# Kernel optimization log

Measured on AMD Instinct MI355X. Metric: run time of the kernel, lower is better.

The kernel has to match this reference:

```python
import jax, jax.numpy as jnp
import numpy as np
from jax import lax

B, L, DM = 2, 1024, 1024
DIN, DSTATE, DCONV, DTRANK = 2048, 16, 4, 64


def setup_inputs() -> dict:
    key = jax.random.key(0)
    ks = jax.random.split(key, 8)
    s = 0.02
    x = jax.random.normal(ks[0], (B, L, DM), jnp.float32)
    in_proj_w = jax.random.normal(ks[1], (2 * DIN, DM), jnp.float32) * s
    conv_w = jax.random.normal(ks[2], (DIN, 1, DCONV), jnp.float32) * 0.2
    conv_b = jnp.zeros((DIN,), jnp.float32)
    x_proj_w = jax.random.normal(ks[3], (DTRANK + 2 * DSTATE, DIN), jnp.float32) * s
    dt_proj_w = jax.random.normal(ks[4], (DIN, DTRANK), jnp.float32) * s
    dt_proj_b = jnp.full((DIN,), -4.0, jnp.float32)  # small init dt after softplus
    # S4D-real init: A_log = log(1..d_state) per channel
    A_log = jnp.log(jnp.broadcast_to(jnp.arange(1, DSTATE + 1, dtype=jnp.float32), (DIN, DSTATE)))
    D_skip = jnp.ones((DIN,), jnp.float32)
    out_proj_w = jax.random.normal(ks[5], (DM, DIN), jnp.float32) * s
    return {
        "x": x, "norm_w": jnp.ones((DM,), jnp.float32), "norm_b": jnp.zeros((DM,), jnp.float32),
        "in_proj_w": in_proj_w, "conv_w": conv_w, "conv_b": conv_b,
        "x_proj_w": x_proj_w, "dt_proj_w": dt_proj_w, "dt_proj_b": dt_proj_b,
        "A_log": A_log, "D_skip": D_skip, "out_proj_w": out_proj_w,
    }


def _layernorm(x, w, b, eps=1e-5):
    mu = jnp.mean(x, axis=-1, keepdims=True)
    var = jnp.mean(jnp.square(x - mu), axis=-1, keepdims=True)
    return (x - mu) * lax.rsqrt(var + eps) * w + b


def _mamba(h, in_proj_w, conv_w, conv_b, x_proj_w, dt_proj_w, dt_proj_b, A_log, D_skip, out_proj_w):
    # h: [B, L, DM]
    xz = jnp.einsum('bld,ed->ble', h, in_proj_w)          # [B, L, 2*DIN]
    xm, z = jnp.split(xz, 2, axis=-1)                     # each [B, L, DIN]
    # causal depthwise conv1d over time
    xc = jnp.transpose(xm, (0, 2, 1))                     # [B, DIN, L]
    xc = jnp.pad(xc, ((0, 0), (0, 0), (DCONV - 1, 0)))
    xc = lax.conv_general_dilated(xc, conv_w, (1,), 'VALID',
                                  dimension_numbers=('NCH', 'OIH', 'NCH'),
                                  feature_group_count=DIN)
    xc = xc + conv_b[None, :, None]
    xc = jnp.transpose(xc, (0, 2, 1))                     # [B, L, DIN]
    xc = jax.nn.silu(xc)
    # input-dependent SSM parameters
    x_dbl = jnp.einsum('bld,ed->ble', xc, x_proj_w)       # [B, L, DTRANK+2N]
    dt, Bm, Cm = jnp.split(x_dbl, [DTRANK, DTRANK + DSTATE], axis=-1)
    dt = jax.nn.softplus(jnp.einsum('blr,dr->bld', dt, dt_proj_w) + dt_proj_b)  # [B, L, DIN]
    A = -jnp.exp(A_log)                                   # [DIN, N]
    deltaA = jnp.exp(dt[..., None] * A)                   # [B, L, DIN, N]
    deltaBu = dt[..., None] * Bm[:, :, None, :] * xc[..., None]  # [B, L, DIN, N]
    # sequential selective scan over time
    dA_t = jnp.transpose(deltaA, (1, 0, 2, 3))            # [L, B, DIN, N]
    dBu_t = jnp.transpose(deltaBu, (1, 0, 2, 3))
    C_t = jnp.transpose(Cm, (1, 0, 2))                    # [L, B, N]

    def step(hs, inp):
        dA, dBu, Ct = inp
        hs = dA * hs + dBu                                # [B, DIN, N]
        y = jnp.einsum('bdn,bn->bd', hs, Ct)
        return hs, y

    h0 = jnp.zeros((B, DIN, DSTATE), xc.dtype)
    _, ys = lax.scan(step, h0, (dA_t, dBu_t, C_t))        # ys: [L, B, DIN]
    y = jnp.transpose(ys, (1, 0, 2)) + xc * D_skip        # [B, L, DIN]
    y = y * jax.nn.silu(z)
    return jnp.einsum('bld,ed->ble', y, out_proj_w)       # [B, L, DM]


def reference(x, norm_w, norm_b, in_proj_w, conv_w, conv_b, x_proj_w,
              dt_proj_w, dt_proj_b, A_log, D_skip, out_proj_w):
    h = _layernorm(x, norm_w, norm_b)
    return x + _mamba(h, in_proj_w, conv_w, conv_b, x_proj_w,
                      dt_proj_w, dt_proj_b, A_log, D_skip, out_proj_w)
```

## Files before the change

### kernel.cpp

```cpp
#include <hip/hip_runtime.h>


typedef unsigned short u16;
typedef unsigned int u32;

typedef __bf16 bf16x8 __attribute__((ext_vector_type(8)));
typedef float f32x4 __attribute__((ext_vector_type(4)));

#define SCAN_G 32
#define SCAN_T 32
#define NSTATE 65536

#if __has_builtin(__builtin_amdgcn_exp2f)
#define EXP2F(x) __builtin_amdgcn_exp2f(x)
#else
#define EXP2F(x) exp2f(x)
#endif
#define LOG2E 1.44269504f

__device__ __forceinline__ u16 f2bf(float f) {
  u32 u = __float_as_uint(f);
  u32 r = u + 0x7FFFu + ((u >> 16) & 1u);
  return (u16)(r >> 16);
}
__device__ __forceinline__ float bf2f(u16 v) {
  return __uint_as_float(((u32)v) << 16);
}

__device__ __forceinline__ void lds_load16(const u16* g, u16* l) {
  __builtin_amdgcn_global_load_lds(
      (const __attribute__((address_space(1))) u32*)g,
      (__attribute__((address_space(3))) u32*)l, 16, 0, 0);
}

__global__ __launch_bounds__(256) void convert_all_kernel(
    const float* __restrict__ w0, const float* __restrict__ w1,
    const float* __restrict__ w2, const float* __restrict__ w3,
    u16* __restrict__ o0, u16* __restrict__ o1,
    u16* __restrict__ o2, u16* __restrict__ o3) {
  const int i = blockIdx.x * 256 + threadIdx.x;
  if (i < 4194304) {
    o0[i] = f2bf(w0[i]);
  } else if (i < 4390912) {
    const int j = i - 4194304;
    o1[j] = f2bf(w1[j]);
  } else if (i < 4521984) {
    const int j = i - 4390912;
    o2[j] = f2bf(w2[j]);
  } else if (i < 6619136) {
    const int j = i - 4521984;
    o3[j] = f2bf(w3[j]);
  }
}

__global__ __launch_bounds__(256) void ln_bf16_kernel(
    const float* __restrict__ x, const float* __restrict__ w,
    const float* __restrict__ b, u16* __restrict__ h) {
  const int row = blockIdx.x;
  const int tid = threadIdx.x;
  const float4 v = ((const float4*)(x + (size_t)row * 1024))[tid];
  float s = v.x + v.y + v.z + v.w;
  float s2 = v.x * v.x + v.y * v.y + v.z * v.z + v.w * v.w;
  for (int off = 32; off >= 1; off >>= 1) {
    s += __shfl_xor(s, off);
    s2 += __shfl_xor(s2, off);
  }
  __shared__ float red[8];
  const int wave = tid >> 6;
  if ((tid & 63) == 0) { red[wave * 2] = s; red[wave * 2 + 1] = s2; }
  __syncthreads();
  s = red[0] + red[2] + red[4] + red[6];
  s2 = red[1] + red[3] + red[5] + red[7];
  const float mu = s * (1.0f / 1024.0f);
  const float var = s2 * (1.0f / 1024.0f) - mu * mu;
  const float rstd = rsqrtf(var + 1e-5f);
  const float4 wv = ((const float4*)w)[tid];
  const float4 bv = ((const float4*)b)[tid];
  ushort4 o;
  o.x = f2bf((v.x - mu) * rstd * wv.x + bv.x);
  o.y = f2bf((v.y - mu) * rstd * wv.y + bv.y);
  o.z = f2bf((v.z - mu) * rstd * wv.z + bv.z);
  o.w = f2bf((v.w - mu) * rstd * wv.w + bv.w);
  ((ushort4*)(h + (size_t)row * 1024))[tid] = o;
}

template <int EPI, int SPLITK>
__global__ __launch_bounds__(256) void gemm_bt(
    const u16* __restrict__ A, const u16* __restrict__ W,
    void* __restrict__ C, const float* __restrict__ extra,
    int M, int N, int K) {
  const int n0 = blockIdx.x * 64;
  const int m0 = blockIdx.y * 64;
  const int ks = (SPLITK > 1) ? blockIdx.z : 0;
  const int kLen = K / SPLITK;
  const int kOff = ks * kLen;
  __shared__ u16 As[64 * 32];
  __shared__ u16 Ws[64 * 32];
  const int tid = threadIdx.x;
  const int wave = tid >> 6;
  const int lane = tid & 63;
  const int wm = (wave >> 1) * 32;
  const int wn = (wave & 1) * 32;
  const int lrow = tid >> 2;
  const int lcg = (tid & 3) * 8;
  const int arow = m0 + lrow;
  const int wrow = n0 + lrow;
  f32x4 acc[2][2];
#pragma unroll
  for (int i = 0; i < 2; ++i)
#pragma unroll
    for (int j = 0; j < 2; ++j) acc[i][j] = (f32x4){0.f, 0.f, 0.f, 0.f};

  const int fm = lane & 15;
  const int fk = (lane >> 4) * 8;

  for (int k0 = kOff; k0 < kOff + kLen; k0 += 32) {
    uint4 av = *(const uint4*)(A + (size_t)arow * K + k0 + lcg);
    uint4 wv = make_uint4(0u, 0u, 0u, 0u);
    if (wrow < N) wv = *(const uint4*)(W + (size_t)wrow * K + k0 + lcg);
    __syncthreads();
    *(uint4*)(As + lrow * 32 + lcg) = av;
    *(uint4*)(Ws + lrow * 32 + lcg) = wv;
    __syncthreads();
    bf16x8 a0 = *(const bf16x8*)(As + (wm + fm) * 32 + fk);
    bf16x8 a1 = *(const bf16x8*)(As + (wm + 16 + fm) * 32 + fk);
    bf16x8 b0 = *(const bf16x8*)(Ws + (wn + fm) * 32 + fk);
    bf16x8 b1 = *(const bf16x8*)(Ws + (wn + 16 + fm) * 32 + fk);
    acc[0][0] = __builtin_amdgcn_mfma_f32_16x16x32_bf16(a0, b0, acc[0][0], 0, 0, 0);
    acc[0][1] = __builtin_amdgcn_mfma_f32_16x16x32_bf16(a0, b1, acc[0][1], 0, 0, 0);
    acc[1][0] = __builtin_amdgcn_mfma_f32_16x16x32_bf16(a1, b0, acc[1][0], 0, 0, 0);
    acc[1][1] = __builtin_amdgcn_mfma_f32_16x16x32_bf16(a1, b1, acc[1][1], 0, 0, 0);
  }

  const int col = lane & 15;
  const int rbase = (lane >> 4) * 4;
#pragma unroll
  for (int tm = 0; tm < 2; ++tm)
#pragma unroll
    for (int tn = 0; tn < 2; ++tn)
#pragma unroll
      for (int r = 0; r < 4; ++r) {
        int m = m0 + wm + tm * 16 + rbase + r;
        int n = n0 + wn + tn * 16 + col;
        if (n < N) {
          float v = acc[tm][tn][r];
          if (EPI == 0) {
            ((float*)C)[(size_t)ks * M * N + (size_t)m * N + n] = v;
          } else {
            v += extra[n];
            v = (v > 20.f) ? v : log1pf(__expf(v));
            ((u16*)C)[(size_t)m * N + n] = f2bf(v);
          }
        }
      }
}

template <int EPI, int SPLITK>
__global__ __launch_bounds__(256) void gemm128_kernel(
    const u16* __restrict__ A, const u16* __restrict__ W,
    u16* __restrict__ Cout, int M, int N, int K) {
  const int n0 = blockIdx.x * 128;
  const int m0 = blockIdx.y * 128;
  const int ks = (SPLITK > 1) ? blockIdx.z : 0;
  const int kLen = K / SPLITK;
  const int k0 = ks * kLen;
  __shared__ u16 As[128 * 32];
  __shared__ u16 Ws[128 * 32];
  const int tid = threadIdx.x;
  const int wave = tid >> 6;
  const int lane = tid & 63;
  const int wm = (wave >> 1) * 64;
  const int wn = (wave & 1) * 64;
  f32x4 acc[4][4];
#pragma unroll
  for (int i = 0; i < 4; ++i)
#pragma unroll
    for (int j = 0; j < 4; ++j) acc[i][j] = (f32x4){0.f, 0.f, 0.f, 0.f};

  const int fm = lane & 15;
  const int fk = (lane >> 4) * 8;
  const int sr = lane >> 2;
  const int sc = (lane & 3) * 8;
  const u16* gA = A + (size_t)(m0 + wave * 32 + sr) * K + k0 + sc;
  const u16* gB = W + (size_t)(n0 + wave * 32 + sr) * K + k0 + sc;
  u16* lA = As + wave * 1024;
  u16* lB = Ws + wave * 1024;

  for (int kk = 0; kk < kLen; kk += 32) {
    __syncthreads();
    lds_load16(gA + kk, lA);
    lds_load16(gA + (size_t)16 * K + kk, lA + 512);
    lds_load16(gB + kk, lB);
    lds_load16(gB + (size_t)16 * K + kk, lB + 512);
    __syncthreads();
    bf16x8 af[4], bfr[4];
#pragma unroll
    for (int i = 0; i < 4; ++i)
      af[i] = *(const bf16x8*)(As + (wm + i * 16 + fm) * 32 + fk);
#pragma unroll
    for (int j = 0; j < 4; ++j)
      bfr[j] = *(const bf16x8*)(Ws + (wn + j * 16 + fm) * 32 + fk);
#pragma unroll
    for (int i = 0; i < 4; ++i)
#pragma unroll
      for (int j = 0; j < 4; ++j)
        acc[i][j] = __builtin_amdgcn_mfma_f32_16x16x32_bf16(af[i], bfr[j], acc[i][j], 0, 0, 0);
  }

  const int col = lane & 15;
  const int rb = (lane >> 4) * 4;
#pragma unroll
  for (int i = 0; i < 4; ++i)
#pragma unroll
    for (int j = 0; j < 4; ++j)
#pragma unroll
      for (int r = 0; r < 4; ++r) {
        const int m = m0 + wm + i * 16 + rb + r;
        const int n = n0 + wn + j * 16 + col;
        if (EPI == 4)
          Cout[(size_t)m * N + n] = f2bf(acc[i][j][r]);
        else
          Cout[(size_t)ks * M * N + (size_t)m * N + n] = f2bf(acc[i][j][r]);
      }
}

__global__ __launch_bounds__(256) void xproj_comb_kernel(
    const float* __restrict__ part, float* __restrict__ xdbl,
    u16* __restrict__ dtr) {
  const int i = blockIdx.x * 256 + threadIdx.x;
  const float v = part[i] + part[i + 196608] + part[i + 2 * 196608] +
                  part[i + 3 * 196608];
  xdbl[i] = v;
  const int m = i / 96;
  const int c = i - m * 96;
  if (c < 64) dtr[(size_t)m * 64 + c] = f2bf(v);
}

__global__ __launch_bounds__(256) void out_comb_kernel(
    const u16* __restrict__ part, const float* __restrict__ x,
    float* __restrict__ out) {
  const int i4 = (blockIdx.x * 256 + threadIdx.x) * 4;
  const float4 xv = *(const float4*)&x[i4];
  float a0 = xv.x, a1 = xv.y, a2 = xv.z, a3 = xv.w;
#pragma unroll
  for (int ks = 0; ks < 4; ++ks) {
    ushort4 pv = *(const ushort4*)&part[(size_t)ks * 2097152 + i4];
    a0 += bf2f(pv.x); a1 += bf2f(pv.y); a2 += bf2f(pv.z); a3 += bf2f(pv.w);
  }
  float4 o = {a0, a1, a2, a3};
  *(float4*)&out[i4] = o;
}

__global__ __launch_bounds__(256) void conv_silu_kernel(
    const u16* __restrict__ xzb, const float* __restrict__ cw,
    const float* __restrict__ cb, u16* __restrict__ xcb) {
  const int idx = blockIdx.x * 256 + threadIdx.x;
  const int d = idx & 2047;
  const int m = idx >> 11;
  const int l = m & 1023;
  const float4 wv = ((const float4*)cw)[d];
  const float w4[4] = {wv.x, wv.y, wv.z, wv.w};
  float acc = cb[d];
#pragma unroll
  for (int k = 0; k < 4; ++k) {
    int lk = l + k - 3;
    if (lk >= 0) acc += bf2f(xzb[(size_t)(m + k - 3) * 4096 + d]) * w4[k];
  }
  const float sv = acc / (1.0f + __expf(-acc));
  xcb[idx] = f2bf(sv);
}


__global__ __launch_bounds__(256) void scan_pass1_kernel(
    const u16* __restrict__ dtb, const u16* __restrict__ xcb,
    const float* __restrict__ xdbl, const float* __restrict__ A_log,
    float* __restrict__ hend, float* __restrict__ prodA) {
  const int bx = blockIdx.x;
  const int d0 = (bx & 7) * 256;
  const int b = (bx >> 3) & 1;
  const int g = bx >> 4;
  const int tid = threadIdx.x;
  const int d = d0 + tid;
  const int mb = b * 1024 + g * SCAN_T;

  float a2[16];
#pragma unroll
  for (int q = 0; q < 4; ++q) {
    float4 al = *(const float4*)&A_log[(size_t)d * 16 + q * 4];
    a2[q * 4 + 0] = -__expf(al.x) * LOG2E;
    a2[q * 4 + 1] = -__expf(al.y) * LOG2E;
    a2[q * 4 + 2] = -__expf(al.z) * LOG2E;
    a2[q * 4 + 3] = -__expf(al.w) * LOG2E;
  }

  __shared__ u32 sdx[SCAN_T][256];

#pragma unroll
  for (int i = tid * 4; i < SCAN_T * 256; i += 1024) {
    const int s = i >> 8, dl = i & 255;
    ushort4 d4 = *(const ushort4*)&dtb[(size_t)(mb + s) * 2048 + d0 + dl];
    ushort4 x4 = *(const ushort4*)&xcb[(size_t)(mb + s) * 2048 + d0 + dl];
    uint4 pk;
    pk.x = (u32)d4.x | ((u32)x4.x << 16);
    pk.y = (u32)d4.y | ((u32)x4.y << 16);
    pk.z = (u32)d4.z | ((u32)x4.z << 16);
    pk.w = (u32)d4.w | ((u32)x4.w << 16);
    *(uint4*)&sdx[s][dl] = pk;
  }
  __syncthreads();

  float h[16];
#pragma unroll
  for (int n = 0; n < 16; ++n) h[n] = 0.f;
  float cs = 0.f;

  for (int s = 0; s < SCAN_T; ++s) {
    const u32 u = sdx[s][tid];
    const float dtv = __uint_as_float(u << 16);
    const float xcv = __uint_as_float(u & 0xFFFF0000u);
    const float du = dtv * xcv;
    const float* Brow = xdbl + (size_t)(mb + s) * 96 + 64;
    const float4 B0 = *(const float4*)(Brow + 0);
    const float4 B1 = *(const float4*)(Brow + 4);
    const float4 B2 = *(const float4*)(Brow + 8);
    const float4 B3 = *(const float4*)(Brow + 12);
    const float Bv[16] = {B0.x, B0.y, B0.z, B0.w, B1.x, B1.y, B1.z, B1.w,
                          B2.x, B2.y, B2.z, B2.w, B3.x, B3.y, B3.z, B3.w};
#pragma unroll
    for (int n = 0; n < 16; ++n) {
      const float da = EXP2F(dtv * a2[n]);
      h[n] = __builtin_fmaf(da, h[n], du * Bv[n]);
    }
    cs += dtv;
  }

  const size_t base = ((size_t)(g * 2 + b) * 2048 + d) * 16;
#pragma unroll
  for (int q = 0; q < 4; ++q) {
    float4 hv = {h[q * 4], h[q * 4 + 1], h[q * 4 + 2], h[q * 4 + 3]};
    *(float4*)&hend[base + q * 4] = hv;
    float4 pv = {EXP2F(a2[q * 4] * cs), EXP2F(a2[q * 4 + 1] * cs),
                 EXP2F(a2[q * 4 + 2] * cs), EXP2F(a2[q * 4 + 3] * cs)};
    *(float4*)&prodA[base + q * 4] = pv;
  }
}

__global__ __launch_bounds__(256) void scan_combine_kernel(
    const float* __restrict__ hend, const float* __restrict__ prodA,
    float* __restrict__ hinit) {
  const int sid = blockIdx.x * 256 + threadIdx.x;
  float H = 0.f;
#pragma unroll 8
  for (int g = 0; g < SCAN_G; ++g) {
    hinit[g * NSTATE + sid] = H;
    H = prodA[g * NSTATE + sid] * H + hend[g * NSTATE + sid];
  }
}

__global__ __launch_bounds__(256) void scan_pass2_kernel(
    const u16* __restrict__ dtb, const u16* __restrict__ xcb,
    const u16* __restrict__ xzb, const float* __restrict__ xdbl,
    const float* __restrict__ A_log, const float* __restrict__ Dsk,
    const float* __restrict__ hinit, u16* __restrict__ yb) {
  const int bx = blockIdx.x;
  const int d0 = (bx & 7) * 256;
  const int b = (bx >> 3) & 1;
  const int g = bx >> 4;
  const int tid = threadIdx.x;
  const int d = d0 + tid;
  const int mb = b * 1024 + g * SCAN_T;

  float a2[16];
#pragma unroll
  for (int q = 0; q < 4; ++q) {
    float4 al = *(const float4*)&A_log[(size_t)d * 16 + q * 4];
    a2[q * 4 + 0] = -__expf(al.x) * LOG2E;
    a2[q * 4 + 1] = -__expf(al.y) * LOG2E;
    a2[q * 4 + 2] = -__expf(al.z) * LOG2E;
    a2[q * 4 + 3] = -__expf(al.w) * LOG2E;
  }
  const float Dd = Dsk[d];

  __shared__ u32 sdx[SCAN_T][256];
  __shared__ u16 sz[SCAN_T][256];

#pragma unroll
  for (int i = tid * 4; i < SCAN_T * 256; i += 1024) {
    const int s = i >> 8, dl = i & 255;
    ushort4 d4 = *(const ushort4*)&dtb[(size_t)(mb + s) * 2048 + d0 + dl];
    ushort4 x4 = *(const ushort4*)&xcb[(size_t)(mb + s) * 2048 + d0 + dl];
    uint4 pk;
    pk.x = (u32)d4.x | ((u32)x4.x << 16);
    pk.y = (u32)d4.y | ((u32)x4.y << 16);
    pk.z = (u32)d4.z | ((u32)x4.z << 16);
    pk.w = (u32)d4.w | ((u32)x4.w << 16);
    *(uint4*)&sdx[s][dl] = pk;
    *(ushort4*)&sz[s][dl] =
        *(const ushort4*)&xzb[(size_t)(mb + s) * 4096 + 2048 + d0 + dl];
  }
  __syncthreads();

  float h[16];
  {
    const float* hi = hinit + ((size_t)(g * 2 + b) * 2048 + d) * 16;
#pragma unroll
    for (int q = 0; q < 4; ++q) {
      float4 hv = *(const float4*)(hi + q * 4);
      h[q * 4] = hv.x; h[q * 4 + 1] = hv.y; h[q * 4 + 2] = hv.z; h[q * 4 + 3] = hv.w;
    }
  }

  for (int s = 0; s < SCAN_T; ++s) {
    const u32 u = sdx[s][tid];
    const float dtv = __uint_as_float(u << 16);
    const float xcv = __uint_as_float(u & 0xFFFF0000u);
    const float du = dtv * xcv;
    const float* Xrow = xdbl + (size_t)(mb + s) * 96 + 64;
    const float4 B0 = *(const float4*)(Xrow + 0);
    const float4 B1 = *(const float4*)(Xrow + 4);
    const float4 B2 = *(const float4*)(Xrow + 8);
    const float4 B3 = *(const float4*)(Xrow + 12);
    const float4 C0 = *(const float4*)(Xrow + 16);
    const float4 C1 = *(const float4*)(Xrow + 20);
    const float4 C2 = *(const float4*)(Xrow + 24);
    const float4 C3 = *(const float4*)(Xrow + 28);
    const float Bv[16] = {B0.x, B0.y, B0.z, B0.w, B1.x, B1.y, B1.z, B1.w,
                          B2.x, B2.y, B2.z, B2.w, B3.x, B3.y, B3.z, B3.w};
    const float Cv[16] = {C0.x, C0.y, C0.z, C0.w, C1.x, C1.y, C1.z, C1.w,
                          C2.x, C2.y, C2.z, C2.w, C3.x, C3.y, C3.z, C3.w};
    float y = 0.f;
#pragma unroll
    for (int n = 0; n < 16; ++n) {
      const float da = EXP2F(dtv * a2[n]);
      h[n] = __builtin_fmaf(da, h[n], du * Bv[n]);
      y = __builtin_fmaf(h[n], Cv[n], y);
    }
    const float zv = bf2f(sz[s][tid]);
    const float sig = 1.0f / (1.0f + EXP2F(-zv * LOG2E));
    const float yv = (y + xcv * Dd) * (zv * sig);
    yb[(size_t)(mb + s) * 2048 + d] = f2bf(yv);
  }
}

extern "C" void kernel_launch(void* const* d_in, const int* in_sizes, int n_in,
                              void* d_out, int out_size, void* d_ws, size_t ws_size,
                              hipStream_t stream) {
  const float* x        = (const float*)d_in[0];
  const float* norm_w   = (const float*)d_in[1];
  const float* norm_b   = (const float*)d_in[2];
  const float* in_projw = (const float*)d_in[3];
  const float* conv_w   = (const float*)d_in[4];
  const float* conv_b   = (const float*)d_in[5];
  const float* x_projw  = (const float*)d_in[6];
  const float* dt_projw = (const float*)d_in[7];
  const float* dt_projb = (const float*)d_in[8];
  const float* A_log    = (const float*)d_in[9];
  const float* D_skip   = (const float*)d_in[10];
  const float* out_projw= (const float*)d_in[11];
  float* out = (float*)d_out;

  char* p = (char*)d_ws;
  auto alloc = [&](size_t bytes) {
    char* r = p;
    p += (bytes + 255) & ~(size_t)255;
    return r;
  };
  u16* xzb    = (u16*)alloc(2048ULL * 4096 * 2);
  u16* xcb    = (u16*)alloc(2048ULL * 2048 * 2);
  u16* dtb16  = (u16*)alloc(2048ULL * 2048 * 2);
  float* xdbl = (float*)alloc(2048ULL * 96 * 4);
  u16* h_bf   = (u16*)alloc(2048ULL * 1024 * 2);
  u16* ybf    = (u16*)alloc(2048ULL * 2048 * 2);
  u16* dtr    = (u16*)alloc(2048ULL * 64 * 2);
  u16* Wi     = (u16*)alloc(4096ULL * 1024 * 2);
  u16* Wx     = (u16*)alloc(96ULL * 2048 * 2);
  u16* Wdt    = (u16*)alloc(2048ULL * 64 * 2);
  u16* Wo     = (u16*)alloc(1024ULL * 2048 * 2);
  float* hend = (float*)alloc((size_t)SCAN_G * NSTATE * 4);
  float* prodA= (float*)alloc((size_t)SCAN_G * NSTATE * 4);
  float* hinit= (float*)alloc((size_t)SCAN_G * NSTATE * 4);
  float* xpart= (float*)alloc(4ULL * 2048 * 96 * 4);
  u16* opart  = xzb;
  (void)ws_size; (void)in_sizes; (void)n_in; (void)out_size;

  convert_all_kernel<<<25856, 256, 0, stream>>>(in_projw, x_projw, dt_projw,
                                                out_projw, Wi, Wx, Wdt, Wo);

  ln_bf16_kernel<<<2048, 256, 0, stream>>>(x, norm_w, norm_b, h_bf);

  gemm128_kernel<4, 1><<<dim3(32, 16), 256, 0, stream>>>(h_bf, Wi, xzb, 2048, 4096, 1024);

  conv_silu_kernel<<<16384, 256, 0, stream>>>(xzb, conv_w, conv_b, xcb);

  gemm_bt<0, 4><<<dim3(2, 32, 4), 256, 0, stream>>>(xcb, Wx, xpart, nullptr, 2048, 96, 2048);
  xproj_comb_kernel<<<768, 256, 0, stream>>>(xpart, xdbl, dtr);

  gemm_bt<2, 1><<<dim3(32, 32), 256, 0, stream>>>(dtr, Wdt, dtb16, dt_projb, 2048, 2048, 64);

  scan_pass1_kernel<<<512, 256, 0, stream>>>(dtb16, xcb, xdbl, A_log, hend, prodA);
  scan_combine_kernel<<<256, 256, 0, stream>>>(hend, prodA, hinit);
  scan_pass2_kernel<<<512, 256, 0, stream>>>(dtb16, xcb, xzb, xdbl, A_log, D_skip,
                                             hinit, ybf);

  gemm128_kernel<3, 4><<<dim3(8, 16, 4), 256, 0, stream>>>(ybf, Wo, opart, 2048, 1024, 2048);
  out_comb_kernel<<<2048, 256, 0, stream>>>(opart, x, out);
}
```

Measured before the change: 253.9 us.

## Fuse split-K combine into dt GEMM, pack dt/xc for scan, merge convert+LN

Merges the weight conversion and layernorm launches into one kernel. Removes the x_proj combine kernel by reducing the split-K partials inside the dt-projection GEMM, which also writes the B/C columns of xdbl. The dt GEMM epilogue now packs softplus(dt) and xc into one u32 array, so the scan passes read it directly from global memory instead of staging through LDS. In exchange the scan loses its coalesced LDS staging, each dt tile redundantly sums four partials, and the packed buffer is larger.

```diff
diff --git a/kernel.cpp b/kernel.cpp
--- a/kernel.cpp
+++ b/kernel.cpp
@@ -33,31 +33,32 @@
       (__attribute__((address_space(3))) u32*)l, 16, 0, 0);
 }
 
-__global__ __launch_bounds__(256) void convert_all_kernel(
+__global__ __launch_bounds__(256) void convert_ln_kernel(
     const float* __restrict__ w0, const float* __restrict__ w1,
     const float* __restrict__ w2, const float* __restrict__ w3,
     u16* __restrict__ o0, u16* __restrict__ o1,
-    u16* __restrict__ o2, u16* __restrict__ o3) {
-  const int i = blockIdx.x * 256 + threadIdx.x;
-  if (i < 4194304) {
-    o0[i] = f2bf(w0[i]);
-  } else if (i < 4390912) {
-    const int j = i - 4194304;
-    o1[j] = f2bf(w1[j]);
-  } else if (i < 4521984) {
-    const int j = i - 4390912;
-    o2[j] = f2bf(w2[j]);
-  } else if (i < 6619136) {
-    const int j = i - 4521984;
-    o3[j] = f2bf(w3[j]);
-  }
-}
-
-__global__ __launch_bounds__(256) void ln_bf16_kernel(
-    const float* __restrict__ x, const float* __restrict__ w,
-    const float* __restrict__ b, u16* __restrict__ h) {
-  const int row = blockIdx.x;
+    u16* __restrict__ o2, u16* __restrict__ o3,
+    const float* __restrict__ x, const float* __restrict__ nw,
+    const float* __restrict__ nb, u16* __restrict__ h) {
+  const int bx = blockIdx.x;
   const int tid = threadIdx.x;
+  if (bx < 25856) {
+    const int i = bx * 256 + tid;
+    if (i < 4194304) {
+      o0[i] = f2bf(w0[i]);
+    } else if (i < 4390912) {
+      const int j = i - 4194304;
+      o1[j] = f2bf(w1[j]);
+    } else if (i < 4521984) {
+      const int j = i - 4390912;
+      o2[j] = f2bf(w2[j]);
+    } else if (i < 6619136) {
+      const int j = i - 4521984;
+      o3[j] = f2bf(w3[j]);
+    }
+    return;
+  }
+  const int row = bx - 25856;
   const float4 v = ((const float4*)(x + (size_t)row * 1024))[tid];
   float s = v.x + v.y + v.z + v.w;
   float s2 = v.x * v.x + v.y * v.y + v.z * v.z + v.w * v.w;
@@ -74,8 +75,8 @@
   const float mu = s * (1.0f / 1024.0f);
   const float var = s2 * (1.0f / 1024.0f) - mu * mu;
   const float rstd = rsqrtf(var + 1e-5f);
-  const float4 wv = ((const float4*)w)[tid];
-  const float4 bv = ((const float4*)b)[tid];
+  const float4 wv = ((const float4*)nw)[tid];
+  const float4 bv = ((const float4*)nb)[tid];
   ushort4 o;
   o.x = f2bf((v.x - mu) * rstd * wv.x + bv.x);
   o.y = f2bf((v.y - mu) * rstd * wv.y + bv.y);
@@ -84,15 +85,13 @@
   ((ushort4*)(h + (size_t)row * 1024))[tid] = o;
 }
 
-template <int EPI, int SPLITK>
-__global__ __launch_bounds__(256) void gemm_bt(
+__global__ __launch_bounds__(256) void gemm_bt_kernel(
     const u16* __restrict__ A, const u16* __restrict__ W,
-    void* __restrict__ C, const float* __restrict__ extra,
-    int M, int N, int K) {
+    float* __restrict__ C, int M, int N, int K) {
   const int n0 = blockIdx.x * 64;
   const int m0 = blockIdx.y * 64;
-  const int ks = (SPLITK > 1) ? blockIdx.z : 0;
-  const int kLen = K / SPLITK;
+  const int ks = blockIdx.z;
+  const int kLen = K / 4;
   const int kOff = ks * kLen;
   __shared__ u16 As[64 * 32];
   __shared__ u16 Ws[64 * 32];
@@ -142,16 +141,95 @@
       for (int r = 0; r < 4; ++r) {
         int m = m0 + wm + tm * 16 + rbase + r;
         int n = n0 + wn + tn * 16 + col;
-        if (n < N) {
-          float v = acc[tm][tn][r];
-          if (EPI == 0) {
-            ((float*)C)[(size_t)ks * M * N + (size_t)m * N + n] = v;
-          } else {
-            v += extra[n];
-            v = (v > 20.f) ? v : log1pf(__expf(v));
-            ((u16*)C)[(size_t)m * N + n] = f2bf(v);
-          }
-        }
+        if (n < N)
+          C[(size_t)ks * M * N + (size_t)m * N + n] = acc[tm][tn][r];
+      }
+}
+
+__global__ __launch_bounds__(256) void dtgemm_fused_kernel(
+    const float* __restrict__ xpart, const u16* __restrict__ Wdt,
+    const float* __restrict__ bias, const u16* __restrict__ xcb,
+    u32* __restrict__ dxp, float* __restrict__ xdbl) {
+  const int N = 2048, K = 64;
+  const int n0 = blockIdx.x * 64;
+  const int m0 = blockIdx.y * 64;
+  const int tid = threadIdx.x;
+
+  if (blockIdx.x == 0) {
+#pragma unroll
+    for (int j = 0; j < 8; ++j) {
+      const int e = tid * 8 + j;
+      const int r = e >> 5, c = e & 31;
+      const size_t ix = (size_t)(m0 + r) * 96 + 64 + c;
+      xdbl[ix] = xpart[ix] + xpart[ix + 196608] + xpart[ix + 2 * 196608] +
+                 xpart[ix + 3 * 196608];
+    }
+  }
+
+  __shared__ u16 As[64 * 32];
+  __shared__ u16 Ws[64 * 32];
+  const int wave = tid >> 6;
+  const int lane = tid & 63;
+  const int wm = (wave >> 1) * 32;
+  const int wn = (wave & 1) * 32;
+  const int lrow = tid >> 2;
+  const int lcg = (tid & 3) * 8;
+  f32x4 acc[2][2];
+#pragma unroll
+  for (int i = 0; i < 2; ++i)
+#pragma unroll
+    for (int j = 0; j < 2; ++j) acc[i][j] = (f32x4){0.f, 0.f, 0.f, 0.f};
+
+  const int fm = lane & 15;
+  const int fk = (lane >> 4) * 8;
+
+  for (int k0 = 0; k0 < K; k0 += 32) {
+    const size_t ab = (size_t)(m0 + lrow) * 96 + k0 + lcg;
+    float av[8];
+#pragma unroll
+    for (int t = 0; t < 2; ++t) {
+      float4 v0 = *(const float4*)&xpart[ab + t * 4];
+      float4 v1 = *(const float4*)&xpart[ab + 196608 + t * 4];
+      float4 v2 = *(const float4*)&xpart[ab + 2 * 196608 + t * 4];
+      float4 v3 = *(const float4*)&xpart[ab + 3 * 196608 + t * 4];
+      av[t * 4 + 0] = v0.x + v1.x + v2.x + v3.x;
+      av[t * 4 + 1] = v0.y + v1.y + v2.y + v3.y;
+      av[t * 4 + 2] = v0.z + v1.z + v2.z + v3.z;
+      av[t * 4 + 3] = v0.w + v1.w + v2.w + v3.w;
+    }
+    ushort4 ap0, ap1;
+    ap0.x = f2bf(av[0]); ap0.y = f2bf(av[1]); ap0.z = f2bf(av[2]); ap0.w = f2bf(av[3]);
+    ap1.x = f2bf(av[4]); ap1.y = f2bf(av[5]); ap1.z = f2bf(av[6]); ap1.w = f2bf(av[7]);
+    uint4 wv = *(const uint4*)(Wdt + (size_t)(n0 + lrow) * K + k0 + lcg);
+    __syncthreads();
+    *(ushort4*)(As + lrow * 32 + lcg) = ap0;
+    *(ushort4*)(As + lrow * 32 + lcg + 4) = ap1;
+    *(uint4*)(Ws + lrow * 32 + lcg) = wv;
+    __syncthreads();
+    bf16x8 a0 = *(const bf16x8*)(As + (wm + fm) * 32 + fk);
+    bf16x8 a1 = *(const bf16x8*)(As + (wm + 16 + fm) * 32 + fk);
+    bf16x8 b0 = *(const bf16x8*)(Ws + (wn + fm) * 32 + fk);
+    bf16x8 b1 = *(const bf16x8*)(Ws + (wn + 16 + fm) * 32 + fk);
+    acc[0][0] = __builtin_amdgcn_mfma_f32_16x16x32_bf16(a0, b0, acc[0][0], 0, 0, 0);
+    acc[0][1] = __builtin_amdgcn_mfma_f32_16x16x32_bf16(a0, b1, acc[0][1], 0, 0, 0);
+    acc[1][0] = __builtin_amdgcn_mfma_f32_16x16x32_bf16(a1, b0, acc[1][0], 0, 0, 0);
+    acc[1][1] = __builtin_amdgcn_mfma_f32_16x16x32_bf16(a1, b1, acc[1][1], 0, 0, 0);
+  }
+
+  const int col = lane & 15;
+  const int rbase = (lane >> 4) * 4;
+#pragma unroll
+  for (int tm = 0; tm < 2; ++tm)
+#pragma unroll
+    for (int tn = 0; tn < 2; ++tn)
+#pragma unroll
+      for (int r = 0; r < 4; ++r) {
+        const int m = m0 + wm + tm * 16 + rbase + r;
+        const int n = n0 + wn + tn * 16 + col;
+        float v = acc[tm][tn][r] + bias[n];
+        v = (v > 20.f) ? v : log1pf(__expf(v));
+        const u32 xc = xcb[(size_t)m * 2048 + n];
+        dxp[(size_t)m * 2048 + n] = (u32)f2bf(v) | (xc << 16);
       }
 }
 
@@ -224,18 +302,6 @@
       }
 }
 
-__global__ __launch_bounds__(256) void xproj_comb_kernel(
-    const float* __restrict__ part, float* __restrict__ xdbl,
-    u16* __restrict__ dtr) {
-  const int i = blockIdx.x * 256 + threadIdx.x;
-  const float v = part[i] + part[i + 196608] + part[i + 2 * 196608] +
-                  part[i + 3 * 196608];
-  xdbl[i] = v;
-  const int m = i / 96;
-  const int c = i - m * 96;
-  if (c < 64) dtr[(size_t)m * 64 + c] = f2bf(v);
-}
-
 __global__ __launch_bounds__(256) void out_comb_kernel(
     const u16* __restrict__ part, const float* __restrict__ x,
     float* __restrict__ out) {
@@ -270,11 +336,10 @@
   xcb[idx] = f2bf(sv);
 }
 
-
 __global__ __launch_bounds__(256) void scan_pass1_kernel(
-    const u16* __restrict__ dtb, const u16* __restrict__ xcb,
-    const float* __restrict__ xdbl, const float* __restrict__ A_log,
-    float* __restrict__ hend, float* __restrict__ prodA) {
+    const u32* __restrict__ dxp, const float* __restrict__ xdbl,
+    const float* __restrict__ A_log, float* __restrict__ hend,
+    float* __restrict__ prodA) {
   const int bx = blockIdx.x;
   const int d0 = (bx & 7) * 256;
   const int b = (bx >> 3) & 1;
@@ -293,37 +358,24 @@
     a2[q * 4 + 3] = -__expf(al.w) * LOG2E;
   }
 
-  __shared__ u32 sdx[SCAN_T][256];
-
-#pragma unroll
-  for (int i = tid * 4; i < SCAN_T * 256; i += 1024) {
-    const int s = i >> 8, dl = i & 255;
-    ushort4 d4 = *(const ushort4*)&dtb[(size_t)(mb + s) * 2048 + d0 + dl];
-    ushort4 x4 = *(const ushort4*)&xcb[(size_t)(mb + s) * 2048 + d0 + dl];
-    uint4 pk;
-    pk.x = (u32)d4.x | ((u32)x4.x << 16);
-    pk.y = (u32)d4.y | ((u32)x4.y << 16);
-    pk.z = (u32)d4.z | ((u32)x4.z << 16);
-    pk.w = (u32)d4.w | ((u32)x4.w << 16);
-    *(uint4*)&sdx[s][dl] = pk;
-  }
-  __syncthreads();
-
   float h[16];
 #pragma unroll
   for (int n = 0; n < 16; ++n) h[n] = 0.f;
   float cs = 0.f;
 
+  const u32* dp = dxp + (size_t)mb * 2048 + d;
+  const float* xb = xdbl + (size_t)mb * 96 + 64;
+
+#pragma unroll 4
   for (int s = 0; s < SCAN_T; ++s) {
-    const u32 u = sdx[s][tid];
+    const u32 u = dp[(size_t)s * 2048];
     const float dtv = __uint_as_float(u << 16);
     const float xcv = __uint_as_float(u & 0xFFFF0000u);
     const float du = dtv * xcv;
-    const float* Brow = xdbl + (size_t)(mb + s) * 96 + 64;
-    const float4 B0 = *(const float4*)(Brow + 0);
-    const float4 B1 = *(const float4*)(Brow + 4);
-    const float4 B2 = *(const float4*)(Brow + 8);
-    const float4 B3 = *(const float4*)(Brow + 12);
+    const float4 B0 = *(const float4*)(xb + (size_t)s * 96 + 0);
+    const float4 B1 = *(const float4*)(xb + (size_t)s * 96 + 4);
+    const float4 B2 = *(const float4*)(xb + (size_t)s * 96 + 8);
+    const float4 B3 = *(const float4*)(xb + (size_t)s * 96 + 12);
     const float Bv[16] = {B0.x, B0.y, B0.z, B0.w, B1.x, B1.y, B1.z, B1.w,
                           B2.x, B2.y, B2.z, B2.w, B3.x, B3.y, B3.z, B3.w};
 #pragma unroll
@@ -358,10 +410,10 @@
 }
 
 __global__ __launch_bounds__(256) void scan_pass2_kernel(
-    const u16* __restrict__ dtb, const u16* __restrict__ xcb,
-    const u16* __restrict__ xzb, const float* __restrict__ xdbl,
-    const float* __restrict__ A_log, const float* __restrict__ Dsk,
-    const float* __restrict__ hinit, u16* __restrict__ yb) {
+    const u32* __restrict__ dxp, const u16* __restrict__ xzb,
+    const float* __restrict__ xdbl, const float* __restrict__ A_log,
+    const float* __restrict__ Dsk, const float* __restrict__ hinit,
+    u16* __restrict__ yb) {
   const int bx = blockIdx.x;
   const int d0 = (bx & 7) * 256;
   const int b = (bx >> 3) & 1;
@@ -381,25 +433,6 @@
   }
   const float Dd = Dsk[d];
 
-  __shared__ u32 sdx[SCAN_T][256];
-  __shared__ u16 sz[SCAN_T][256];
-
-#pragma unroll
-  for (int i = tid * 4; i < SCAN_T * 256; i += 1024) {
-    const int s = i >> 8, dl = i & 255;
-    ushort4 d4 = *(const ushort4*)&dtb[(size_t)(mb + s) * 2048 + d0 + dl];
-    ushort4 x4 = *(const ushort4*)&xcb[(size_t)(mb + s) * 2048 + d0 + dl];
-    uint4 pk;
-    pk.x = (u32)d4.x | ((u32)x4.x << 16);
-    pk.y = (u32)d4.y | ((u32)x4.y << 16);
-    pk.z = (u32)d4.z | ((u32)x4.z << 16);
-    pk.w = (u32)d4.w | ((u32)x4.w << 16);
-    *(uint4*)&sdx[s][dl] = pk;
-    *(ushort4*)&sz[s][dl] =
-        *(const ushort4*)&xzb[(size_t)(mb + s) * 4096 + 2048 + d0 + dl];
-  }
-  __syncthreads();
-
   float h[16];
   {
     const float* hi = hinit + ((size_t)(g * 2 + b) * 2048 + d) * 16;
@@ -410,20 +443,25 @@
     }
   }
 
+  const u32* dp = dxp + (size_t)mb * 2048 + d;
+  const u16* zp = xzb + (size_t)mb * 4096 + 2048 + d;
+  const float* xb = xdbl + (size_t)mb * 96 + 64;
+  u16* yp = yb + (size_t)mb * 2048 + d;
+
+#pragma unroll 2
   for (int s = 0; s < SCAN_T; ++s) {
-    const u32 u = sdx[s][tid];
+    const u32 u = dp[(size_t)s * 2048];
     const float dtv = __uint_as_float(u << 16);
     const float xcv = __uint_as_float(u & 0xFFFF0000u);
     const float du = dtv * xcv;
-    const float* Xrow = xdbl + (size_t)(mb + s) * 96 + 64;
-    const float4 B0 = *(const float4*)(Xrow + 0);
-    const float4 B1 = *(const float4*)(Xrow + 4);
-    const float4 B2 = *(const float4*)(Xrow + 8);
-    const float4 B3 = *(const float4*)(Xrow + 12);
-    const float4 C0 = *(const float4*)(Xrow + 16);
-    const float4 C1 = *(const float4*)(Xrow + 20);
-    const float4 C2 = *(const float4*)(Xrow + 24);
-    const float4 C3 = *(const float4*)(Xrow + 28);
+    const float4 B0 = *(const float4*)(xb + (size_t)s * 96 + 0);
+    const float4 B1 = *(const float4*)(xb + (size_t)s * 96 + 4);
+    const float4 B2 = *(const float4*)(xb + (size_t)s * 96 + 8);
+    const float4 B3 = *(const float4*)(xb + (size_t)s * 96 + 12);
+    const float4 C0 = *(const float4*)(xb + (size_t)s * 96 + 16);
+    const float4 C1 = *(const float4*)(xb + (size_t)s * 96 + 20);
+    const float4 C2 = *(const float4*)(xb + (size_t)s * 96 + 24);
+    const float4 C3 = *(const float4*)(xb + (size_t)s * 96 + 28);
     const float Bv[16] = {B0.x, B0.y, B0.z, B0.w, B1.x, B1.y, B1.z, B1.w,
                           B2.x, B2.y, B2.z, B2.w, B3.x, B3.y, B3.z, B3.w};
     const float Cv[16] = {C0.x, C0.y, C0.z, C0.w, C1.x, C1.y, C1.z, C1.w,
@@ -435,10 +473,10 @@
       h[n] = __builtin_fmaf(da, h[n], du * Bv[n]);
       y = __builtin_fmaf(h[n], Cv[n], y);
     }
-    const float zv = bf2f(sz[s][tid]);
+    const float zv = bf2f(zp[(size_t)s * 4096]);
     const float sig = 1.0f / (1.0f + EXP2F(-zv * LOG2E));
     const float yv = (y + xcv * Dd) * (zv * sig);
-    yb[(size_t)(mb + s) * 2048 + d] = f2bf(yv);
+    yp[(size_t)s * 2048] = f2bf(yv);
   }
 }
 
@@ -467,11 +505,10 @@
   };
   u16* xzb    = (u16*)alloc(2048ULL * 4096 * 2);
   u16* xcb    = (u16*)alloc(2048ULL * 2048 * 2);
-  u16* dtb16  = (u16*)alloc(2048ULL * 2048 * 2);
+  u32* dxp    = (u32*)alloc(2048ULL * 2048 * 4);
   float* xdbl = (float*)alloc(2048ULL * 96 * 4);
   u16* h_bf   = (u16*)alloc(2048ULL * 1024 * 2);
   u16* ybf    = (u16*)alloc(2048ULL * 2048 * 2);
-  u16* dtr    = (u16*)alloc(2048ULL * 64 * 2);
   u16* Wi     = (u16*)alloc(4096ULL * 1024 * 2);
   u16* Wx     = (u16*)alloc(96ULL * 2048 * 2);
   u16* Wdt    = (u16*)alloc(2048ULL * 64 * 2);
@@ -483,23 +520,22 @@
   u16* opart  = xzb;
   (void)ws_size; (void)in_sizes; (void)n_in; (void)out_size;
 
-  convert_all_kernel<<<25856, 256, 0, stream>>>(in_projw, x_projw, dt_projw,
-                                                out_projw, Wi, Wx, Wdt, Wo);
-
-  ln_bf16_kernel<<<2048, 256, 0, stream>>>(x, norm_w, norm_b, h_bf);
+  convert_ln_kernel<<<27904, 256, 0, stream>>>(in_projw, x_projw, dt_projw,
+                                               out_projw, Wi, Wx, Wdt, Wo,
+                                               x, norm_w, norm_b, h_bf);
 
   gemm128_kernel<4, 1><<<dim3(32, 16), 256, 0, stream>>>(h_bf, Wi, xzb, 2048, 4096, 1024);
 
   conv_silu_kernel<<<16384, 256, 0, stream>>>(xzb, conv_w, conv_b, xcb);
 
-  gemm_bt<0, 4><<<dim3(2, 32, 4), 256, 0, stream>>>(xcb, Wx, xpart, nullptr, 2048, 96, 2048);
-  xproj_comb_kernel<<<768, 256, 0, stream>>>(xpart, xdbl, dtr);
-
-  gemm_bt<2, 1><<<dim3(32, 32), 256, 0, stream>>>(dtr, Wdt, dtb16, dt_projb, 2048, 2048, 64);
-
-  scan_pass1_kernel<<<512, 256, 0, stream>>>(dtb16, xcb, xdbl, A_log, hend, prodA);
+  gemm_bt_kernel<<<dim3(2, 32, 4), 256, 0, stream>>>(xcb, Wx, xpart, 2048, 96, 2048);
+
+  dtgemm_fused_kernel<<<dim3(32, 32), 256, 0, stream>>>(xpart, Wdt, dt_projb,
+                                                        xcb, dxp, xdbl);
+
+  scan_pass1_kernel<<<512, 256, 0, stream>>>(dxp, xdbl, A_log, hend, prodA);
   scan_combine_kernel<<<256, 256, 0, stream>>>(hend, prodA, hinit);
-  scan_pass2_kernel<<<512, 256, 0, stream>>>(dtb16, xcb, xzb, xdbl, A_log, D_skip,
+  scan_pass2_kernel<<<512, 256, 0, stream>>>(dxp, xzb, xdbl, A_log, D_skip,
                                              hinit, ybf);
 
   gemm128_kernel<3, 4><<<dim3(8, 16, 4), 256, 0, stream>>>(ybf, Wo, opart, 2048, 1024, 2048);
```

New measurement: 243.9 us. -4.0%, faster.
